# Kernel optimization log

Measured on AMD Instinct MI355X. Metric: run time of the kernel, lower is better.

The kernel has to match this reference:

```python
import jax, jax.numpy as jnp
import numpy as np

CUTOFF = 5.0
NUM_RBF = 8
POLY_P = 5
AVG_NEIGH = 16.0
NUM_LAYERS = 2
NUM_RANKS = 4  # edge angular ranks 0..3 (Cartesian dims 1,3,9,27)
C = 64


def _radial(edge_vec):
    # r: [E,1]; Bessel-j0 basis with polynomial cutoff envelope (MACE-style)
    r = jnp.sqrt(jnp.sum(edge_vec * edge_vec, axis=-1, keepdims=True) + 1e-12)
    x = r / CUTOFF
    p = float(POLY_P)
    env = (1.0 - 0.5 * (p + 1.0) * (p + 2.0) * x**POLY_P
           + p * (p + 2.0) * x**(POLY_P + 1)
           - 0.5 * p * (p + 1.0) * x**(POLY_P + 2))
    env = jnp.where(x < 1.0, env, 0.0)
    k = jnp.arange(1, NUM_RBF + 1, dtype=edge_vec.dtype)
    basis = jnp.sqrt(2.0 / CUTOFF) * jnp.sin(k * jnp.pi * x) / r  # [E,K]
    return basis * env, r


def _angular(rhat):
    # Cartesian ICTD-style angular basis, ranks 0..3, norm constants sqrt(2r+1)
    E = rhat.shape[0]
    y0 = jnp.ones((E, 1), rhat.dtype)
    y1 = jnp.sqrt(3.0) * rhat  # [E,3]
    o2 = rhat[:, :, None] * rhat[:, None, :]
    y2 = jnp.sqrt(5.0) * o2.reshape(E, 9)
    o3 = o2[:, :, :, None] * rhat[:, None, None, :]
    y3 = jnp.sqrt(7.0) * o3.reshape(E, 27)
    return (y0, y1, y2, y3)


def setup_inputs() -> dict:
    key = jax.random.key(0)
    ks = jax.random.split(key, 12)
    N, E = 5000, 80000
    species = jax.random.randint(ks[0], (N,), 0, 10, dtype=jnp.int32)
    senders = jax.random.randint(ks[1], (E,), 0, N, dtype=jnp.int32)
    receivers = jax.random.randint(ks[2], (E,), 0, N, dtype=jnp.int32)
    edge_vec = 1.5 * jax.random.normal(ks[3], (E, 3), jnp.float32)
    embed_w = jax.random.normal(ks[4], (10, C), jnp.float32)
    rad_w1 = jax.random.normal(ks[5], (NUM_LAYERS, NUM_RBF, 64), jnp.float32) / np.sqrt(NUM_RBF)
    rad_w2 = jax.random.normal(ks[6], (NUM_LAYERS, 64, 64), jnp.float32) / 8.0
    rad_w3 = jax.random.normal(ks[7], (NUM_LAYERS, 64, 64), jnp.float32) / 8.0
    rad_w4 = jax.random.normal(ks[8], (NUM_LAYERS, 64, NUM_RANKS * C), jnp.float32) / 8.0
    mix_w = jax.random.normal(ks[9], (NUM_LAYERS, NUM_RANKS, C, C), jnp.float32) / 8.0
    read_w = jax.random.normal(ks[10], (NUM_LAYERS, C), jnp.float32) / 8.0
    return {"species": species, "senders": senders, "receivers": receivers,
            "edge_vec": edge_vec, "embed_w": embed_w, "rad_w1": rad_w1,
            "rad_w2": rad_w2, "rad_w3": rad_w3, "rad_w4": rad_w4,
            "mix_w": mix_w, "read_w": read_w}


def reference(species, senders, receivers, edge_vec, embed_w,
              rad_w1, rad_w2, rad_w3, rad_w4, mix_w, read_w):
    N = species.shape[0]
    E = edge_vec.shape[0]
    rb, r = _radial(edge_vec)                      # [E,K]
    rhat = edge_vec / r
    Y = _angular(rhat)                             # tuple of [E,dim_r]
    h0 = embed_w[species]                          # [N,C] species embedding
    node_energy = jnp.zeros((N,), edge_vec.dtype)
    for l in range(NUM_LAYERS):
        # radial MLP -> per-rank, per-channel edge weights [E, NUM_RANKS, C]
        h = jax.nn.silu(rb @ rad_w1[l])
        h = jax.nn.silu(h @ rad_w2[l])
        h = jax.nn.silu(h @ rad_w3[l])
        R = (h @ rad_w4[l]).reshape(E, NUM_RANKS, C)
        hj = h0[senders]                           # neighbor gather [E,C]
        h0_new = jnp.zeros_like(h0)
        for ri in range(NUM_RANKS):
            # equivariant edge tensor product: radial * scalar feat x angular
            m = (R[:, ri, :] * hj)[:, :, None] * Y[ri][:, None, :]  # [E,C,dim]
            A = jax.ops.segment_sum(m, receivers, num_segments=N) / AVG_NEIGH
            if ri == 0:
                h0_new = h0_new + A[..., 0] @ mix_w[l, 0]
            else:
                # correlation-2 invariant contraction of equivariant features
                h0_new = h0_new + jnp.einsum('ncd,ncd->nc', A, A) @ mix_w[l, ri]
        node_energy = node_energy + h0_new @ read_w[l]
        h0 = h0_new
    return node_energy
```

## Files before the change

### kernel.cpp

```cpp
#include <hip/hip_runtime.h>
#include <math.h>


#define PI_F 3.14159265358979323846f
#define LOG2E_F 1.44269504088896340736f

typedef _Float16 f16x8 __attribute__((ext_vector_type(8)));
typedef float f32x4 __attribute__((ext_vector_type(4)));

union FU { uint4 u; f16x8 h; };

__device__ __forceinline__ float silu_f(float x) {
    float e = __builtin_amdgcn_exp2f(-LOG2E_F * x);
    return x * __builtin_amdgcn_rcpf(1.0f + e);
}

__device__ __forceinline__ uint pack2_f16(float a, float b) {
    return __builtin_bit_cast(uint, __builtin_amdgcn_cvt_pkrtz(a, b));
}

__device__ __forceinline__ float unpk_f16(uint u, int hi) {
    unsigned short s = hi ? (unsigned short)(u >> 16) : (unsigned short)(u & 0xffff);
    return (float)__builtin_bit_cast(_Float16, s);
}

__global__ void k_setup(const float* __restrict__ rw1,
                        const float* __restrict__ rw2,
                        const float* __restrict__ rw3,
                        const float* __restrict__ rw4,
                        uint* __restrict__ Wf1, uint* __restrict__ Wf2,
                        uint* __restrict__ Wf3, uint* __restrict__ Wf4,
                        const int* __restrict__ species,
                        const float* __restrict__ embw,
                        float* __restrict__ h0,
                        int* __restrict__ counts, int* __restrict__ cursor,
                        int N, int NC)
{
    int tid = blockIdx.x * blockDim.x + threadIdx.x;
    if (tid < N) { counts[tid] = 0; cursor[tid] = 0; }
    if (tid < NC) {
        int n = tid >> 6, c = tid & 63;
        h0[tid] = embw[species[n]*64 + c];
    }
    if (tid < 2048) {
        int reg = tid & 3, lane = (tid >> 2) & 63, ot = (tid >> 8) & 3, l = tid >> 10;
        int out = 16*ot + (lane & 15);
        int k   = 8*(lane >> 4) + 2*reg;
        float lo = (k   < 8) ? rw1[l*512 + k*64 + out]     : 0.0f;
        float hi = (k+1 < 8) ? rw1[l*512 + (k+1)*64 + out] : 0.0f;
        Wf1[tid] = pack2_f16(lo, hi);
    }
    if (tid >= 2048 && tid < 2048 + 4096) {
        int t = tid - 2048;
        int reg = t & 3, lane = (t >> 2) & 63, kt = (t >> 8) & 1, ot = (t >> 9) & 3, l = t >> 11;
        int out = 16*ot + (lane & 15);
        int k   = 32*kt + 8*(lane >> 4) + 2*reg;
        Wf2[t] = pack2_f16(rw2[l*4096 + k*64 + out], rw2[l*4096 + (k+1)*64 + out]);
    }
    if (tid >= 6144 && tid < 6144 + 4096) {
        int t = tid - 6144;
        int reg = t & 3, lane = (t >> 2) & 63, kt = (t >> 8) & 1, ot = (t >> 9) & 3, l = t >> 11;
        int out = 16*ot + (lane & 15);
        int k   = 32*kt + 8*(lane >> 4) + 2*reg;
        Wf3[t] = pack2_f16(rw3[l*4096 + k*64 + out], rw3[l*4096 + (k+1)*64 + out]);
    }
    if (tid >= 10240 && tid < 10240 + 16384) {
        int t = tid - 10240;
        int reg = t & 3, lane = (t >> 2) & 63, kt = (t >> 8) & 1, ot = (t >> 9) & 15, l = t >> 13;
        int out = 16*ot + (lane & 15);
        int k   = 32*kt + 8*(lane >> 4) + 2*reg;
        Wf4[t] = pack2_f16(rw4[l*16384 + k*256 + out], rw4[l*16384 + (k+1)*256 + out]);
    }
}

__global__ void k_edge_basis(const float* __restrict__ ev,
                             const int* __restrict__ recv,
                             uint*  __restrict__ rbh,
                             float* __restrict__ rhat4,
                             int*   __restrict__ counts,
                             int E)
{
    int e = blockIdx.x * blockDim.x + threadIdx.x;
    if (e >= E) return;
    float vx = ev[3*e+0], vy = ev[3*e+1], vz = ev[3*e+2];
    float r2 = vx*vx + vy*vy + vz*vz + 1e-12f;
    float r  = sqrtf(r2);
    float x  = r * 0.2f;
    float x2 = x*x;
    float x5 = x2*x2*x;
    float env = 1.0f + x5*(-21.0f + x*(35.0f - 15.0f*x));
    if (x >= 1.0f) env = 0.0f;
    float pref = 0.632455532033675866f / r * env;
    float pix  = PI_F * x;
    float bas[8];
    #pragma unroll
    for (int k = 0; k < 8; ++k) bas[k] = pref * __sinf((float)(k+1) * pix);
    uint* o = rbh + (size_t)e*4;
    #pragma unroll
    for (int k = 0; k < 4; ++k) o[k] = pack2_f16(bas[2*k], bas[2*k+1]);

    float ir = 1.0f / r;
    float4 rh;
    rh.x = vx*ir; rh.y = vy*ir; rh.z = vz*ir; rh.w = 0.0f;
    *(float4*)(rhat4 + (size_t)e*4) = rh;

    atomicAdd(&counts[recv[e]], 1);
}

__global__ void k_scan(const int* __restrict__ counts, int* __restrict__ offsets, int N)
{
    __shared__ int wsum[16];
    __shared__ int basev;
    int lane = threadIdx.x & 63;
    int w    = threadIdx.x >> 6;
    if (threadIdx.x == 0) basev = 0;
    __syncthreads();
    for (int start = 0; start < N; start += 1024) {
        int i = start + (int)threadIdx.x;
        int v = (i < N) ? counts[i] : 0;
        int s = v;
        #pragma unroll
        for (int off = 1; off < 64; off <<= 1) {
            int t = __shfl_up(s, off, 64);
            if (lane >= off) s += t;
        }
        if (lane == 63) wsum[w] = s;
        __syncthreads();
        int wbase = 0;
        {
            int ws = (lane < 16) ? wsum[lane] : 0;
            #pragma unroll
            for (int off = 1; off < 16; off <<= 1) {
                int t = __shfl_up(ws, off, 64);
                if (lane >= off) ws += t;
            }
            int excl = __shfl(ws, w - 1, 64);
            wbase = (w == 0) ? 0 : excl;
        }
        if (i < N) offsets[i] = basev + wbase + s - v;
        __syncthreads();
        if (threadIdx.x == 1023) basev += wbase + s;
        __syncthreads();
    }
    if (threadIdx.x == 0) offsets[N] = basev;
}

__global__ void k_scatter(const int* __restrict__ recv,
                          const int* __restrict__ offsets,
                          int* __restrict__ cursor,
                          int* __restrict__ elist, int E)
{
    int e = blockIdx.x * blockDim.x + threadIdx.x;
    if (e >= E) return;
    int r = recv[e];
    int p = atomicAdd(&cursor[r], 1);
    elist[offsets[r] + p] = e;
}

__global__ __launch_bounds__(256) void k_sort_perm(
    const int* __restrict__ offsets,
    int* __restrict__ elist,
    const int* __restrict__ senders,
    const float* __restrict__ rhat4,
    int* __restrict__ eslot,
    int* __restrict__ csr_send,
    float* __restrict__ csr_rhat,
    int N)
{
    int lane = threadIdx.x & 63;
    int node = (blockIdx.x * blockDim.x + threadIdx.x) >> 6;
    if (node >= N) return;
    int beg = offsets[node], end = offsets[node+1];
    int d = end - beg;
    if (d <= 0) return;
    if (d <= 64) {
        int v = (lane < d) ? elist[beg + lane] : 0x7fffffff;
        int rank = 0;
        #pragma unroll 8
        for (int j = 0; j < 64; ++j) {
            int vj = __shfl(v, j, 64);
            rank += (vj < v) ? 1 : 0;
        }
        if (lane < d) {
            int slot = beg + rank;
            eslot[v] = slot;
            csr_send[slot] = senders[v];
            *(float4*)(csr_rhat + (size_t)slot*4) = *(const float4*)(rhat4 + (size_t)v*4);
        }
    } else {
        if (lane == 0) {
            for (int i = beg + 1; i < end; ++i) {
                int v = elist[i];
                int j = i - 1;
                while (j >= beg && elist[j] > v) { elist[j+1] = elist[j]; --j; }
                elist[j+1] = v;
            }
            for (int s = beg; s < end; ++s) {
                int e = elist[s];
                eslot[e] = s;
                csr_send[s] = senders[e];
                *(float4*)(csr_rhat + (size_t)s*4) = *(const float4*)(rhat4 + (size_t)e*4);
            }
        }
    }
}

__global__ __launch_bounds__(128) void k_mlp_mfma(
    const uint* __restrict__ rbh,
    const uint* __restrict__ Wf1, const uint* __restrict__ Wf2,
    const uint* __restrict__ Wf3, const uint* __restrict__ Wf4,
    const int* __restrict__ eslot,
    uint* __restrict__ Rpk,
    int E, int tiles)
{
    __shared__ __align__(16) uint Hl[2][32][132];
    int lane = threadIdx.x & 63;
    int w    = threadIdx.x >> 6;
    int wid  = blockIdx.x * 2 + w;
    if (wid >= 2 * tiles) return;
    int l    = wid / tiles;
    int tile = wid % tiles;
    int e0   = tile * 32;

    uint (*H)[132] = Hl[w];
    int er = lane & 15;
    int kb = lane >> 4;

    f32x4 zero4 = {0.f, 0.f, 0.f, 0.f};

    FU b0, b1;
    b0.u = make_uint4(0,0,0,0);
    b1.u = make_uint4(0,0,0,0);
    if (kb == 0) {
        int ea = e0 + er, eb = e0 + 16 + er;
        if (ea < E) b0.u = *(const uint4*)(rbh + (size_t)ea*4);
        if (eb < E) b1.u = *(const uint4*)(rbh + (size_t)eb*4);
    }
    f32x4 d0[4], d1[4];
    #pragma unroll
    for (int ot = 0; ot < 4; ++ot) {
        FU a;
        a.u = *(const uint4*)(Wf1 + ((size_t)(l*4 + ot)*64 + lane)*4);
        d0[ot] = __builtin_amdgcn_mfma_f32_16x16x32_f16(a.h, b0.h, zero4, 0, 0, 0);
        d1[ot] = __builtin_amdgcn_mfma_f32_16x16x32_f16(a.h, b1.h, zero4, 0, 0, 0);
    }
    #pragma unroll
    for (int ot = 0; ot < 4; ++ot) {
        uint* dA = &H[er][8*ot + 2*kb];
        dA[0] = pack2_f16(silu_f(d0[ot][0]), silu_f(d0[ot][1]));
        dA[1] = pack2_f16(silu_f(d0[ot][2]), silu_f(d0[ot][3]));
        uint* dB = &H[16 + er][8*ot + 2*kb];
        dB[0] = pack2_f16(silu_f(d1[ot][0]), silu_f(d1[ot][1]));
        dB[1] = pack2_f16(silu_f(d1[ot][2]), silu_f(d1[ot][3]));
    }

    const uint* Wfs[2] = { Wf2, Wf3 };
    #pragma unroll
    for (int s = 0; s < 2; ++s) {
        FU hA0, hA1, hB0, hB1;
        hA0.u = *(const uint4*)&H[er][4*kb];
        hA1.u = *(const uint4*)&H[er][16 + 4*kb];
        hB0.u = *(const uint4*)&H[16 + er][4*kb];
        hB1.u = *(const uint4*)&H[16 + er][16 + 4*kb];
        #pragma unroll
        for (int ot = 0; ot < 4; ++ot) {
            FU a;
            a.u = *(const uint4*)(Wfs[s] + ((size_t)((l*4 + ot)*2 + 0)*64 + lane)*4);
            d0[ot] = __builtin_amdgcn_mfma_f32_16x16x32_f16(a.h, hA0.h, zero4, 0, 0, 0);
            d1[ot] = __builtin_amdgcn_mfma_f32_16x16x32_f16(a.h, hB0.h, zero4, 0, 0, 0);
            a.u = *(const uint4*)(Wfs[s] + ((size_t)((l*4 + ot)*2 + 1)*64 + lane)*4);
            d0[ot] = __builtin_amdgcn_mfma_f32_16x16x32_f16(a.h, hA1.h, d0[ot], 0, 0, 0);
            d1[ot] = __builtin_amdgcn_mfma_f32_16x16x32_f16(a.h, hB1.h, d1[ot], 0, 0, 0);
        }
        #pragma unroll
        for (int ot = 0; ot < 4; ++ot) {
            uint* dA = &H[er][8*ot + 2*kb];
            dA[0] = pack2_f16(silu_f(d0[ot][0]), silu_f(d0[ot][1]));
            dA[1] = pack2_f16(silu_f(d0[ot][2]), silu_f(d0[ot][3]));
            uint* dB = &H[16 + er][8*ot + 2*kb];
            dB[0] = pack2_f16(silu_f(d1[ot][0]), silu_f(d1[ot][1]));
            dB[1] = pack2_f16(silu_f(d1[ot][2]), silu_f(d1[ot][3]));
        }
    }

    FU hA0, hA1, hB0, hB1;
    hA0.u = *(const uint4*)&H[er][4*kb];
    hA1.u = *(const uint4*)&H[er][16 + 4*kb];
    hB0.u = *(const uint4*)&H[16 + er][4*kb];
    hB1.u = *(const uint4*)&H[16 + er][16 + 4*kb];
    #pragma unroll
    for (int ri = 0; ri < 4; ++ri) {
        #pragma unroll
        for (int otl = 0; otl < 4; ++otl) {
            int ot = ri*4 + otl;
            FU a;
            f32x4 dA, dB;
            a.u = *(const uint4*)(Wf4 + ((size_t)((l*16 + ot)*2 + 0)*64 + lane)*4);
            dA = __builtin_amdgcn_mfma_f32_16x16x32_f16(a.h, hA0.h, zero4, 0, 0, 0);
            dB = __builtin_amdgcn_mfma_f32_16x16x32_f16(a.h, hB0.h, zero4, 0, 0, 0);
            a.u = *(const uint4*)(Wf4 + ((size_t)((l*16 + ot)*2 + 1)*64 + lane)*4);
            dA = __builtin_amdgcn_mfma_f32_16x16x32_f16(a.h, hA1.h, dA, 0, 0, 0);
            dB = __builtin_amdgcn_mfma_f32_16x16x32_f16(a.h, hB1.h, dB, 0, 0, 0);
            int p = otl*8 + kb*2;
            H[er][(p  )*4 + ri] = pack2_f16(dA[0], dA[1]);
            H[er][(p+1)*4 + ri] = pack2_f16(dA[2], dA[3]);
            H[16 + er][(p  )*4 + ri] = pack2_f16(dB[0], dB[1]);
            H[16 + er][(p+1)*4 + ri] = pack2_f16(dB[2], dB[3]);
        }
    }
    #pragma unroll
    for (int it = 0; it < 16; ++it) {
        int f   = it*64 + lane;
        int row = f >> 5;
        int q4  = (f & 31) * 4;
        int eg  = e0 + row;
        if (eg < E) {
            int slot = eslot[eg];
            *(uint4*)(Rpk + ((size_t)l*E + slot)*128 + q4) = *(const uint4*)&H[row][q4];
        }
    }
}

__global__ __launch_bounds__(256) void k_node(
    const uint*  __restrict__ Rpk,
    const float* __restrict__ h0,
    const int*   __restrict__ csr_send,
    const float* __restrict__ csr_rhat,
    const int*   __restrict__ offsets,
    const float* __restrict__ mixw,
    const float* __restrict__ readw,
    float* __restrict__ h0n,
    const float* __restrict__ eprev,
    float* __restrict__ eout,
    int N)
{
    int gtid = blockIdx.x * blockDim.x + threadIdx.x;
    int wave = gtid >> 6;
    int lane = threadIdx.x & 63;
    int w    = threadIdx.x >> 6;
    __shared__ float Bl[4][4][64];
    bool active = (wave < N);
    int n = active ? wave : 0;
    int half  = lane & 1;
    int cpair = lane >> 1;

    float a0 = 0.f;
    float a1[3]  = {0.f,0.f,0.f};
    float a2[6]  = {0.f,0.f,0.f,0.f,0.f,0.f};
    float a3[10] = {0.f,0.f,0.f,0.f,0.f,0.f,0.f,0.f,0.f,0.f};

    auto accum = [&](float x, float y, float z, float hj, uint4 qv) {
        float t0 = unpk_f16(qv.x, half) * hj;
        float t1 = unpk_f16(qv.y, half) * hj;
        float t2 = unpk_f16(qv.z, half) * hj;
        float t3 = unpk_f16(qv.w, half) * hj;
        a0 += t0;
        a1[0] = fmaf(t1, x, a1[0]);
        a1[1] = fmaf(t1, y, a1[1]);
        a1[2] = fmaf(t1, z, a1[2]);
        float qxx = x*x, qxy = x*y, qxz = x*z, qyy = y*y, qyz = y*z, qzz = z*z;
        a2[0] = fmaf(t2, qxx, a2[0]);
        a2[1] = fmaf(t2, qxy, a2[1]);
        a2[2] = fmaf(t2, qxz, a2[2]);
        a2[3] = fmaf(t2, qyy, a2[3]);
        a2[4] = fmaf(t2, qyz, a2[4]);
        a2[5] = fmaf(t2, qzz, a2[5]);
        float u0 = t3*qxx, u1 = t3*qxy, u3 = t3*qyy, u5 = t3*qzz;
        a3[0] = fmaf(u0, x, a3[0]);
        a3[1] = fmaf(u0, y, a3[1]);
        a3[2] = fmaf(u0, z, a3[2]);
        a3[3] = fmaf(u3, x, a3[3]);
        a3[4] = fmaf(u1, z, a3[4]);
        a3[5] = fmaf(u5, x, a3[5]);
        a3[6] = fmaf(u3, y, a3[6]);
        a3[7] = fmaf(u3, z, a3[7]);
        a3[8] = fmaf(u5, y, a3[8]);
        a3[9] = fmaf(u5, z, a3[9]);
    };

    if (active) {
        int beg = __builtin_amdgcn_readfirstlane(offsets[n]);
        int end = __builtin_amdgcn_readfirstlane(offsets[n+1]);
        int i = beg;
        for (; i + 4 <= end; i += 4) {
            int sn_[4]; float4 rh_[4]; float hj_[4]; uint4 q_[4];
            #pragma unroll
            for (int k = 0; k < 4; ++k) sn_[k] = csr_send[i+k];
            #pragma unroll
            for (int k = 0; k < 4; ++k) {
                rh_[k] = *(const float4*)(csr_rhat + (size_t)(i+k)*4);
                q_[k]  = *(const uint4*)(Rpk + (size_t)(i+k)*128 + cpair*4);
            }
            #pragma unroll
            for (int k = 0; k < 4; ++k) hj_[k] = h0[(size_t)sn_[k]*64 + lane];
            #pragma unroll
            for (int k = 0; k < 4; ++k)
                accum(rh_[k].x, rh_[k].y, rh_[k].z, hj_[k], q_[k]);
        }
        for (; i < end; ++i) {
            int snd = csr_send[i];
            float4 rh = *(const float4*)(csr_rhat + (size_t)i*4);
            uint4  qv = *(const uint4*)(Rpk + (size_t)i*128 + cpair*4);
            float  hj = h0[(size_t)snd*64 + lane];
            accum(rh.x, rh.y, rh.z, hj, qv);
        }
    }

    float B0 = a0 * 0.0625f;
    float s1 = a1[0]*a1[0] + a1[1]*a1[1] + a1[2]*a1[2];
    float B1 = s1 * (3.0f/256.0f);
    float s2 = a2[0]*a2[0] + a2[3]*a2[3] + a2[5]*a2[5]
             + 2.0f*(a2[1]*a2[1] + a2[2]*a2[2] + a2[4]*a2[4]);
    float B2 = s2 * (5.0f/256.0f);
    float s3 = a3[0]*a3[0] + a3[6]*a3[6] + a3[9]*a3[9]
             + 3.0f*(a3[1]*a3[1] + a3[2]*a3[2] + a3[3]*a3[3]
                   + a3[5]*a3[5] + a3[7]*a3[7] + a3[8]*a3[8])
             + 6.0f*a3[4]*a3[4];
    float B3 = s3 * (7.0f/256.0f);

    Bl[w][0][lane] = B0;
    Bl[w][1][lane] = B1;
    Bl[w][2][lane] = B2;
    Bl[w][3][lane] = B3;
    __syncthreads();

    if (active) {
        float acc = 0.0f;
        for (int ri = 0; ri < 4; ++ri) {
            #pragma unroll 8
            for (int j = 0; j < 64; ++j)
                acc = fmaf(Bl[w][ri][j], mixw[(ri*64 + j)*64 + lane], acc);
        }
        h0n[(size_t)n*64 + lane] = acc;

        float evl = acc * readw[lane];
        #pragma unroll
        for (int off = 1; off < 64; off <<= 1) evl += __shfl_xor(evl, off, 64);
        if (lane == 0) {
            float o = evl;
            if (eprev) o += eprev[n];
            eout[n] = o;
        }
    }
}

extern "C" void kernel_launch(void* const* d_in, const int* in_sizes, int n_in,
                              void* d_out, int out_size, void* d_ws, size_t ws_size,
                              hipStream_t stream)
{
    const int*   species   = (const int*)  d_in[0];
    const int*   senders   = (const int*)  d_in[1];
    const int*   receivers = (const int*)  d_in[2];
    const float* edge_vec  = (const float*)d_in[3];
    const float* embed_w   = (const float*)d_in[4];
    const float* rad_w1    = (const float*)d_in[5];
    const float* rad_w2    = (const float*)d_in[6];
    const float* rad_w3    = (const float*)d_in[7];
    const float* rad_w4    = (const float*)d_in[8];
    const float* mix_w     = (const float*)d_in[9];
    const float* read_w    = (const float*)d_in[10];

    int N = in_sizes[0];
    int E = in_sizes[1];
    float* out = (float*)d_out;

    char* ws = (char*)d_ws;
    size_t off = 0;
    auto alloc = [&](size_t bytes) -> char* {
        char* p = ws + off;
        off = (off + bytes + 255) & ~(size_t)255;
        return p;
    };
    uint*  rbh     = (uint*) alloc((size_t)E*4*sizeof(uint));
    float* rhat4   = (float*)alloc((size_t)E*4*sizeof(float));
    float* h0a     = (float*)alloc((size_t)N*64*sizeof(float));
    float* h0b     = (float*)alloc((size_t)N*64*sizeof(float));
    float* ener    = (float*)alloc((size_t)N*sizeof(float));
    int* counts    = (int*)alloc((size_t)N*sizeof(int));
    int* offsets   = (int*)alloc((size_t)(N+1)*sizeof(int));
    int* cursor    = (int*)alloc((size_t)N*sizeof(int));
    int* elist     = (int*)alloc((size_t)E*sizeof(int));
    int* eslot     = (int*)alloc((size_t)E*sizeof(int));
    int* csr_send  = (int*)alloc((size_t)E*sizeof(int));
    float* csr_rhat= (float*)alloc((size_t)E*4*sizeof(float));
    uint* Wf1      = (uint*)alloc(2048*sizeof(uint));
    uint* Wf2      = (uint*)alloc(4096*sizeof(uint));
    uint* Wf3      = (uint*)alloc(4096*sizeof(uint));
    uint* Wf4      = (uint*)alloc(16384*sizeof(uint));
    uint* Rpk      = (uint*)alloc((size_t)2*E*128*sizeof(uint));

    int NC = N * 64;
    k_setup<<<(NC + 255)/256, 256, 0, stream>>>(
        rad_w1, rad_w2, rad_w3, rad_w4, Wf1, Wf2, Wf3, Wf4,
        species, embed_w, h0a, counts, cursor, N, NC);

    k_edge_basis<<<(E + 255)/256, 256, 0, stream>>>(
        edge_vec, receivers, rbh, rhat4, counts, E);
    k_scan<<<1, 1024, 0, stream>>>(counts, offsets, N);
    k_scatter<<<(E + 255)/256, 256, 0, stream>>>(receivers, offsets, cursor, elist, E);
    k_sort_perm<<<((size_t)N*64 + 255)/256, 256, 0, stream>>>(
        offsets, elist, senders, rhat4, eslot, csr_send, csr_rhat, N);

    int tiles = (E + 31) / 32;
    int waves = 2 * tiles;
    k_mlp_mfma<<<(waves + 1)/2, 128, 0, stream>>>(
        rbh, Wf1, Wf2, Wf3, Wf4, eslot, Rpk, E, tiles);

    float* hcur = h0a;
    float* hnxt = h0b;
    for (int l = 0; l < 2; ++l) {
        uint* Rl = Rpk + (size_t)l * E * 128;
        k_node<<<((size_t)N*64 + 255)/256, 256, 0, stream>>>(
            Rl, hcur, csr_send, csr_rhat, offsets,
            mix_w + (size_t)l*4*64*64,
            read_w + (size_t)l*64,
            hnxt,
            (l == 0) ? nullptr : ener,
            (l == 0) ? ener : out,
            N);
        float* tmp = hcur; hcur = hnxt; hnxt = tmp;
    }
}
```

Before: 112.9 us.

## Permute radial basis into CSR order and pre-gather sender features per layer

The sort kernel now writes the radial basis in CSR slot order, so the MLP kernel reads and writes Rpk contiguously instead of scattering through an eslot indirection. A new per-layer kernel gathers sender node features into a dense CSR-ordered buffer, which k_node then reads without dependent index loads. This removes the scattered Rpk writes and the index-then-gather latency chain in k_node. In exchange it adds two extra launches and writes and rereads a 20 MB feature buffer per layer.

Result: slower. 132.3 us (+17.2%).

```diff
diff --git a/kernel.cpp b/kernel.cpp
--- a/kernel.cpp
+++ b/kernel.cpp
@@ -162,9 +162,10 @@
     int* __restrict__ elist,
     const int* __restrict__ senders,
     const float* __restrict__ rhat4,
-    int* __restrict__ eslot,
+    const uint* __restrict__ rbh,
     int* __restrict__ csr_send,
     float* __restrict__ csr_rhat,
+    uint* __restrict__ csr_rbh,
     int N)
 {
     int lane = threadIdx.x & 63;
@@ -183,9 +184,9 @@
         }
         if (lane < d) {
             int slot = beg + rank;
-            eslot[v] = slot;
             csr_send[slot] = senders[v];
             *(float4*)(csr_rhat + (size_t)slot*4) = *(const float4*)(rhat4 + (size_t)v*4);
+            *(uint4*)(csr_rbh + (size_t)slot*4)   = *(const uint4*)(rbh + (size_t)v*4);
         }
     } else {
         if (lane == 0) {
@@ -197,19 +198,28 @@
             }
             for (int s = beg; s < end; ++s) {
                 int e = elist[s];
-                eslot[e] = s;
                 csr_send[s] = senders[e];
                 *(float4*)(csr_rhat + (size_t)s*4) = *(const float4*)(rhat4 + (size_t)e*4);
+                *(uint4*)(csr_rbh + (size_t)s*4)   = *(const uint4*)(rbh + (size_t)e*4);
             }
         }
     }
 }
 
+__global__ void k_gather_hj(const float* __restrict__ h0,
+                            const int* __restrict__ csr_send,
+                            float* __restrict__ csr_hj, int total)
+{
+    int t = blockIdx.x * blockDim.x + threadIdx.x;
+    if (t >= total) return;
+    int slot = t >> 6, c = t & 63;
+    csr_hj[t] = h0[(size_t)csr_send[slot]*64 + c];
+}
+
 __global__ __launch_bounds__(128) void k_mlp_mfma(
-    const uint* __restrict__ rbh,
+    const uint* __restrict__ csr_rbh,
     const uint* __restrict__ Wf1, const uint* __restrict__ Wf2,
     const uint* __restrict__ Wf3, const uint* __restrict__ Wf4,
-    const int* __restrict__ eslot,
     uint* __restrict__ Rpk,
     int E, int tiles)
 {
@@ -233,8 +243,8 @@
     b1.u = make_uint4(0,0,0,0);
     if (kb == 0) {
         int ea = e0 + er, eb = e0 + 16 + er;
-        if (ea < E) b0.u = *(const uint4*)(rbh + (size_t)ea*4);
-        if (eb < E) b1.u = *(const uint4*)(rbh + (size_t)eb*4);
+        if (ea < E) b0.u = *(const uint4*)(csr_rbh + (size_t)ea*4);
+        if (eb < E) b1.u = *(const uint4*)(csr_rbh + (size_t)eb*4);
     }
     f32x4 d0[4], d1[4];
     #pragma unroll
@@ -314,17 +324,14 @@
         int row = f >> 5;
         int q4  = (f & 31) * 4;
         int eg  = e0 + row;
-        if (eg < E) {
-            int slot = eslot[eg];
-            *(uint4*)(Rpk + ((size_t)l*E + slot)*128 + q4) = *(const uint4*)&H[row][q4];
-        }
+        if (eg < E)
+            *(uint4*)(Rpk + ((size_t)l*E + eg)*128 + q4) = *(const uint4*)&H[row][q4];
     }
 }
 
 __global__ __launch_bounds__(256) void k_node(
     const uint*  __restrict__ Rpk,
-    const float* __restrict__ h0,
-    const int*   __restrict__ csr_send,
+    const float* __restrict__ csr_hj,
     const float* __restrict__ csr_rhat,
     const int*   __restrict__ offsets,
     const float* __restrict__ mixw,
@@ -383,25 +390,21 @@
         int end = __builtin_amdgcn_readfirstlane(offsets[n+1]);
         int i = beg;
         for (; i + 4 <= end; i += 4) {
-            int sn_[4]; float4 rh_[4]; float hj_[4]; uint4 q_[4];
-            #pragma unroll
-            for (int k = 0; k < 4; ++k) sn_[k] = csr_send[i+k];
+            float4 rh_[4]; float hj_[4]; uint4 q_[4];
             #pragma unroll
             for (int k = 0; k < 4; ++k) {
                 rh_[k] = *(const float4*)(csr_rhat + (size_t)(i+k)*4);
                 q_[k]  = *(const uint4*)(Rpk + (size_t)(i+k)*128 + cpair*4);
+                hj_[k] = csr_hj[(size_t)(i+k)*64 + lane];
             }
-            #pragma unroll
-            for (int k = 0; k < 4; ++k) hj_[k] = h0[(size_t)sn_[k]*64 + lane];
             #pragma unroll
             for (int k = 0; k < 4; ++k)
                 accum(rh_[k].x, rh_[k].y, rh_[k].z, hj_[k], q_[k]);
         }
         for (; i < end; ++i) {
-            int snd = csr_send[i];
             float4 rh = *(const float4*)(csr_rhat + (size_t)i*4);
             uint4  qv = *(const uint4*)(Rpk + (size_t)i*128 + cpair*4);
-            float  hj = h0[(size_t)snd*64 + lane];
+            float  hj = csr_hj[(size_t)i*64 + lane];
             accum(rh.x, rh.y, rh.z, hj, qv);
         }
     }
@@ -480,9 +483,10 @@
     int* offsets   = (int*)alloc((size_t)(N+1)*sizeof(int));
     int* cursor    = (int*)alloc((size_t)N*sizeof(int));
     int* elist     = (int*)alloc((size_t)E*sizeof(int));
-    int* eslot     = (int*)alloc((size_t)E*sizeof(int));
     int* csr_send  = (int*)alloc((size_t)E*sizeof(int));
     float* csr_rhat= (float*)alloc((size_t)E*4*sizeof(float));
+    uint* csr_rbh  = (uint*)alloc((size_t)E*4*sizeof(uint));
+    float* csr_hj  = (float*)alloc((size_t)E*64*sizeof(float));
     uint* Wf1      = (uint*)alloc(2048*sizeof(uint));
     uint* Wf2      = (uint*)alloc(4096*sizeof(uint));
     uint* Wf3      = (uint*)alloc(4096*sizeof(uint));
@@ -499,19 +503,21 @@
     k_scan<<<1, 1024, 0, stream>>>(counts, offsets, N);
     k_scatter<<<(E + 255)/256, 256, 0, stream>>>(receivers, offsets, cursor, elist, E);
     k_sort_perm<<<((size_t)N*64 + 255)/256, 256, 0, stream>>>(
-        offsets, elist, senders, rhat4, eslot, csr_send, csr_rhat, N);
+        offsets, elist, senders, rhat4, rbh, csr_send, csr_rhat, csr_rbh, N);
 
     int tiles = (E + 31) / 32;
     int waves = 2 * tiles;
     k_mlp_mfma<<<(waves + 1)/2, 128, 0, stream>>>(
-        rbh, Wf1, Wf2, Wf3, Wf4, eslot, Rpk, E, tiles);
+        csr_rbh, Wf1, Wf2, Wf3, Wf4, Rpk, E, tiles);
 
     float* hcur = h0a;
     float* hnxt = h0b;
+    int EG = E * 64;
     for (int l = 0; l < 2; ++l) {
         uint* Rl = Rpk + (size_t)l * E * 128;
+        k_gather_hj<<<(EG + 255)/256, 256, 0, stream>>>(hcur, csr_send, csr_hj, EG);
         k_node<<<((size_t)N*64 + 255)/256, 256, 0, stream>>>(
-            Rl, hcur, csr_send, csr_rhat, offsets,
+            Rl, csr_hj, csr_rhat, offsets,
             mix_w + (size_t)l*4*64*64,
             read_w + (size_t)l*64,
             hnxt,
```

## Fuse CSR build stages into one cooperative kernel with grid syncs

Applied to the files above, without the earlier changes.

Replaces the separate edge-basis, scan, scatter and sort-permutation kernels with a single cooperative kernel of 256 blocks that uses grid-wide syncs between phases. The scan becomes a block-partitioned two-level scan instead of a single-block serial loop. The aim is to remove several kernel launch gaps and the slow one-block scan. In exchange, each grid.sync has its own cost and the sort phase runs on far fewer waves than before, so it loses parallelism.

Result: slower. 286.1 us (+153.4%).

```diff
diff --git a/kernel.cpp b/kernel.cpp
--- a/kernel.cpp
+++ b/kernel.cpp
@@ -1,6 +1,9 @@
 #include <hip/hip_runtime.h>
+#include <hip/hip_cooperative_groups.h>
 #include <math.h>
 
+
+namespace cg = cooperative_groups;
 
 #define PI_F 3.14159265358979323846f
 #define LOG2E_F 1.44269504088896340736f
@@ -33,11 +36,9 @@
                         const int* __restrict__ species,
                         const float* __restrict__ embw,
                         float* __restrict__ h0,
-                        int* __restrict__ counts, int* __restrict__ cursor,
-                        int N, int NC)
+                        int NC)
 {
     int tid = blockIdx.x * blockDim.x + threadIdx.x;
-    if (tid < N) { counts[tid] = 0; cursor[tid] = 0; }
     if (tid < NC) {
         int n = tid >> 6, c = tid & 63;
         h0[tid] = embw[species[n]*64 + c];
@@ -73,133 +74,140 @@
     }
 }
 
-__global__ void k_edge_basis(const float* __restrict__ ev,
-                             const int* __restrict__ recv,
-                             uint*  __restrict__ rbh,
-                             float* __restrict__ rhat4,
-                             int*   __restrict__ counts,
-                             int E)
-{
-    int e = blockIdx.x * blockDim.x + threadIdx.x;
-    if (e >= E) return;
-    float vx = ev[3*e+0], vy = ev[3*e+1], vz = ev[3*e+2];
-    float r2 = vx*vx + vy*vy + vz*vz + 1e-12f;
-    float r  = sqrtf(r2);
-    float x  = r * 0.2f;
-    float x2 = x*x;
-    float x5 = x2*x2*x;
-    float env = 1.0f + x5*(-21.0f + x*(35.0f - 15.0f*x));
-    if (x >= 1.0f) env = 0.0f;
-    float pref = 0.632455532033675866f / r * env;
-    float pix  = PI_F * x;
-    float bas[8];
-    #pragma unroll
-    for (int k = 0; k < 8; ++k) bas[k] = pref * __sinf((float)(k+1) * pix);
-    uint* o = rbh + (size_t)e*4;
-    #pragma unroll
-    for (int k = 0; k < 4; ++k) o[k] = pack2_f16(bas[2*k], bas[2*k+1]);
-
-    float ir = 1.0f / r;
-    float4 rh;
-    rh.x = vx*ir; rh.y = vy*ir; rh.z = vz*ir; rh.w = 0.0f;
-    *(float4*)(rhat4 + (size_t)e*4) = rh;
-
-    atomicAdd(&counts[recv[e]], 1);
-}
-
-__global__ void k_scan(const int* __restrict__ counts, int* __restrict__ offsets, int N)
-{
-    __shared__ int wsum[16];
-    __shared__ int basev;
-    int lane = threadIdx.x & 63;
-    int w    = threadIdx.x >> 6;
-    if (threadIdx.x == 0) basev = 0;
-    __syncthreads();
-    for (int start = 0; start < N; start += 1024) {
-        int i = start + (int)threadIdx.x;
-        int v = (i < N) ? counts[i] : 0;
-        int s = v;
-        #pragma unroll
-        for (int off = 1; off < 64; off <<= 1) {
-            int t = __shfl_up(s, off, 64);
-            if (lane >= off) s += t;
-        }
-        if (lane == 63) wsum[w] = s;
-        __syncthreads();
-        int wbase = 0;
-        {
-            int ws = (lane < 16) ? wsum[lane] : 0;
-            #pragma unroll
-            for (int off = 1; off < 16; off <<= 1) {
-                int t = __shfl_up(ws, off, 64);
-                if (lane >= off) ws += t;
-            }
-            int excl = __shfl(ws, w - 1, 64);
-            wbase = (w == 0) ? 0 : excl;
-        }
-        if (i < N) offsets[i] = basev + wbase + s - v;
-        __syncthreads();
-        if (threadIdx.x == 1023) basev += wbase + s;
-        __syncthreads();
-    }
-    if (threadIdx.x == 0) offsets[N] = basev;
-}
-
-__global__ void k_scatter(const int* __restrict__ recv,
-                          const int* __restrict__ offsets,
-                          int* __restrict__ cursor,
-                          int* __restrict__ elist, int E)
-{
-    int e = blockIdx.x * blockDim.x + threadIdx.x;
-    if (e >= E) return;
-    int r = recv[e];
-    int p = atomicAdd(&cursor[r], 1);
-    elist[offsets[r] + p] = e;
-}
-
-__global__ __launch_bounds__(256) void k_sort_perm(
-    const int* __restrict__ offsets,
+__global__ __launch_bounds__(256) void k_csr(
+    const float* __restrict__ ev,
+    const int* __restrict__ recv,
+    const int* __restrict__ senders,
+    uint*  __restrict__ rbh,
+    float* __restrict__ rhat4,
+    int* __restrict__ counts,
+    int* __restrict__ cursor,
+    int* __restrict__ offsets,
     int* __restrict__ elist,
-    const int* __restrict__ senders,
-    const float* __restrict__ rhat4,
+    int* __restrict__ blocksum,
     int* __restrict__ eslot,
     int* __restrict__ csr_send,
     float* __restrict__ csr_rhat,
-    int N)
+    int N, int E)
 {
-    int lane = threadIdx.x & 63;
-    int node = (blockIdx.x * blockDim.x + threadIdx.x) >> 6;
-    if (node >= N) return;
-    int beg = offsets[node], end = offsets[node+1];
-    int d = end - beg;
-    if (d <= 0) return;
-    if (d <= 64) {
-        int v = (lane < d) ? elist[beg + lane] : 0x7fffffff;
-        int rank = 0;
-        #pragma unroll 8
-        for (int j = 0; j < 64; ++j) {
-            int vj = __shfl(v, j, 64);
-            rank += (vj < v) ? 1 : 0;
-        }
-        if (lane < d) {
-            int slot = beg + rank;
-            eslot[v] = slot;
-            csr_send[slot] = senders[v];
-            *(float4*)(csr_rhat + (size_t)slot*4) = *(const float4*)(rhat4 + (size_t)v*4);
-        }
-    } else {
-        if (lane == 0) {
-            for (int i = beg + 1; i < end; ++i) {
-                int v = elist[i];
-                int j = i - 1;
-                while (j >= beg && elist[j] > v) { elist[j+1] = elist[j]; --j; }
-                elist[j+1] = v;
-            }
-            for (int s = beg; s < end; ++s) {
-                int e = elist[s];
-                eslot[e] = s;
-                csr_send[s] = senders[e];
-                *(float4*)(csr_rhat + (size_t)s*4) = *(const float4*)(rhat4 + (size_t)e*4);
+    cg::grid_group grid = cg::this_grid();
+    __shared__ int red[256];
+    int tid  = blockIdx.x * blockDim.x + threadIdx.x;
+    int nthr = gridDim.x * blockDim.x;
+    int G    = gridDim.x;
+    int chunk = (N + G - 1) / G;
+
+    for (int i = tid; i < N; i += nthr) { counts[i] = 0; cursor[i] = 0; }
+    grid.sync();
+
+    for (int e = tid; e < E; e += nthr) {
+        float vx = ev[3*e+0], vy = ev[3*e+1], vz = ev[3*e+2];
+        float r2 = vx*vx + vy*vy + vz*vz + 1e-12f;
+        float r  = sqrtf(r2);
+        float x  = r * 0.2f;
+        float x2 = x*x;
+        float x5 = x2*x2*x;
+        float env = 1.0f + x5*(-21.0f + x*(35.0f - 15.0f*x));
+        if (x >= 1.0f) env = 0.0f;
+        float pref = 0.632455532033675866f / r * env;
+        float pix  = PI_F * x;
+        float bas[8];
+        #pragma unroll
+        for (int k = 0; k < 8; ++k) bas[k] = pref * __sinf((float)(k+1) * pix);
+        uint* o = rbh + (size_t)e*4;
+        #pragma unroll
+        for (int k = 0; k < 4; ++k) o[k] = pack2_f16(bas[2*k], bas[2*k+1]);
+        float ir = 1.0f / r;
+        float4 rh;
+        rh.x = vx*ir; rh.y = vy*ir; rh.z = vz*ir; rh.w = 0.0f;
+        *(float4*)(rhat4 + (size_t)e*4) = rh;
+        atomicAdd(&counts[recv[e]], 1);
+    }
+    grid.sync();
+
+    {
+        int start = blockIdx.x * chunk;
+        int stop  = min(start + chunk, N);
+        int v = 0;
+        for (int i = start + (int)threadIdx.x; i < stop; i += 256) v += counts[i];
+        red[threadIdx.x] = v;
+        __syncthreads();
+        for (int off = 128; off > 0; off >>= 1) {
+            if (threadIdx.x < (unsigned)off) red[threadIdx.x] += red[threadIdx.x + off];
+            __syncthreads();
+        }
+        if (threadIdx.x == 0) blocksum[blockIdx.x] = red[0];
+    }
+    grid.sync();
+
+    if (blockIdx.x == 0) {
+        int t = threadIdx.x;
+        int v = (t < G) ? blocksum[t] : 0;
+        red[t] = v;
+        __syncthreads();
+        for (int off = 1; off < 256; off <<= 1) {
+            int add = (t >= (unsigned)off) ? red[t - off] : 0;
+            __syncthreads();
+            red[t] += add;
+            __syncthreads();
+        }
+        if (t < G) blocksum[t] = (t == 0) ? 0 : red[t-1];
+        if (t == 0) offsets[N] = E;
+    }
+    grid.sync();
+
+    if (threadIdx.x == 0) {
+        int start = blockIdx.x * chunk;
+        int stop  = min(start + chunk, N);
+        int run = blocksum[blockIdx.x];
+        for (int i = start; i < stop; ++i) { offsets[i] = run; run += counts[i]; }
+    }
+    grid.sync();
+
+    for (int e = tid; e < E; e += nthr) {
+        int r = recv[e];
+        int p = atomicAdd(&cursor[r], 1);
+        elist[offsets[r] + p] = e;
+    }
+    grid.sync();
+
+    {
+        int lane   = threadIdx.x & 63;
+        int wid    = (blockIdx.x * 4) + (threadIdx.x >> 6);
+        int nwaves = G * 4;
+        for (int node = wid; node < N; node += nwaves) {
+            int beg = offsets[node], end = offsets[node+1];
+            int d = end - beg;
+            if (d <= 0) continue;
+            if (d <= 64) {
+                int v = (lane < d) ? elist[beg + lane] : 0x7fffffff;
+                int rank = 0;
+                #pragma unroll 8
+                for (int j = 0; j < 64; ++j) {
+                    int vj = __shfl(v, j, 64);
+                    rank += (vj < v) ? 1 : 0;
+                }
+                if (lane < d) {
+                    int slot = beg + rank;
+                    eslot[v] = slot;
+                    csr_send[slot] = senders[v];
+                    *(float4*)(csr_rhat + (size_t)slot*4) = *(const float4*)(rhat4 + (size_t)v*4);
+                }
+            } else {
+                if (lane == 0) {
+                    for (int i = beg + 1; i < end; ++i) {
+                        int v = elist[i];
+                        int j = i - 1;
+                        while (j >= beg && elist[j] > v) { elist[j+1] = elist[j]; --j; }
+                        elist[j+1] = v;
+                    }
+                    for (int s = beg; s < end; ++s) {
+                        int e = elist[s];
+                        eslot[e] = s;
+                        csr_send[s] = senders[e];
+                        *(float4*)(csr_rhat + (size_t)s*4) = *(const float4*)(rhat4 + (size_t)e*4);
+                    }
+                }
             }
         }
     }
@@ -483,6 +491,7 @@
     int* eslot     = (int*)alloc((size_t)E*sizeof(int));
     int* csr_send  = (int*)alloc((size_t)E*sizeof(int));
     float* csr_rhat= (float*)alloc((size_t)E*4*sizeof(float));
+    int* blocksum  = (int*)alloc(256*sizeof(int));
     uint* Wf1      = (uint*)alloc(2048*sizeof(uint));
     uint* Wf2      = (uint*)alloc(4096*sizeof(uint));
     uint* Wf3      = (uint*)alloc(4096*sizeof(uint));
@@ -490,16 +499,23 @@
     uint* Rpk      = (uint*)alloc((size_t)2*E*128*sizeof(uint));
 
     int NC = N * 64;
-    k_setup<<<(NC + 255)/256, 256, 0, stream>>>(
+    k_setup<<<(26624 + 255)/256 > (NC + 255)/256 ? (26624 + 255)/256 : (NC + 255)/256,
+              256, 0, stream>>>(
         rad_w1, rad_w2, rad_w3, rad_w4, Wf1, Wf2, Wf3, Wf4,
-        species, embed_w, h0a, counts, cursor, N, NC);
-
-    k_edge_basis<<<(E + 255)/256, 256, 0, stream>>>(
-        edge_vec, receivers, rbh, rhat4, counts, E);
-    k_scan<<<1, 1024, 0, stream>>>(counts, offsets, N);
-    k_scatter<<<(E + 255)/256, 256, 0, stream>>>(receivers, offsets, cursor, elist, E);
-    k_sort_perm<<<((size_t)N*64 + 255)/256, 256, 0, stream>>>(
-        offsets, elist, senders, rhat4, eslot, csr_send, csr_rhat, N);
+        species, embed_w, h0a, NC);
+
+    {
+        int G = 256;
+        void* args[] = {
+            (void*)&edge_vec, (void*)&receivers, (void*)&senders,
+            (void*)&rbh, (void*)&rhat4,
+            (void*)&counts, (void*)&cursor, (void*)&offsets, (void*)&elist,
+            (void*)&blocksum, (void*)&eslot, (void*)&csr_send, (void*)&csr_rhat,
+            (void*)&N, (void*)&E
+        };
+        hipLaunchCooperativeKernel((const void*)k_csr, dim3(G), dim3(256),
+                                   args, 0, stream);
+    }
 
     int tiles = (E + 31) / 32;
     int waves = 2 * tiles;
```
